# Performance work log

Hardware: AMD Instinct MI355X
Metric: run time of the kernel (lower is better)

The kernel has to match this reference:

```python
import jax, jax.numpy as jnp
import numpy as np

H = 256
V_IN = 32000
V_OUT = 32000
T = 2048


def setup_inputs() -> dict:
    key = jax.random.key(0)
    ks = jax.random.split(key, 16)
    s = 1.0 / np.sqrt(H)
    inp = {
        "src": jax.random.randint(ks[0], (T, 1), 0, V_IN, dtype=jnp.int64 if jax.config.jax_enable_x64 else jnp.int32),
        "trg": jax.random.randint(ks[1], (T, 1), 0, V_OUT, dtype=jnp.int64 if jax.config.jax_enable_x64 else jnp.int32),
        "enc_emb": jax.random.normal(ks[2], (V_IN, H), jnp.float32),
        "enc_W_ih": jax.random.uniform(ks[3], (3 * H, H), jnp.float32, -s, s),
        "enc_W_hh": jax.random.uniform(ks[4], (3 * H, H), jnp.float32, -s, s),
        "enc_b_ih": jax.random.uniform(ks[5], (3 * H,), jnp.float32, -s, s),
        "enc_b_hh": jax.random.uniform(ks[6], (3 * H,), jnp.float32, -s, s),
        "dec_emb": jax.random.normal(ks[7], (V_OUT, H), jnp.float32),
        "dec_W_ih": jax.random.uniform(ks[8], (3 * H, H), jnp.float32, -s, s),
        "dec_W_hh": jax.random.uniform(ks[9], (3 * H, H), jnp.float32, -s, s),
        "dec_b_ih": jax.random.uniform(ks[10], (3 * H,), jnp.float32, -s, s),
        "dec_b_hh": jax.random.uniform(ks[11], (3 * H,), jnp.float32, -s, s),
        "out_W": jax.random.uniform(ks[12], (V_OUT, H), jnp.float32, -s, s),
        "out_b": jax.random.uniform(ks[13], (V_OUT,), jnp.float32, -s, s),
    }
    return inp


def _gru_step(x, h, W_ih, W_hh, b_ih, b_hh):
    # PyTorch GRU cell math. x,h: [H]
    gi = W_ih @ x + b_ih          # [3H]
    gh = W_hh @ h + b_hh          # [3H]
    i_r, i_z, i_n = jnp.split(gi, 3)
    h_r, h_z, h_n = jnp.split(gh, 3)
    r = jax.nn.sigmoid(i_r + h_r)
    z = jax.nn.sigmoid(i_z + h_z)
    n = jnp.tanh(i_n + r * h_n)
    return (1.0 - z) * n + z * h


def reference(src, trg, enc_emb, enc_W_ih, enc_W_hh, enc_b_ih, enc_b_hh,
              dec_emb, dec_W_ih, dec_W_hh, dec_b_ih, dec_b_hh, out_W, out_b):
    src_t = src[:, 0]  # [T], batch forced to 1 by .view(1,1,-1)
    trg_t = trg[:, 0]  # [T]
    h0 = jnp.zeros((H,), enc_emb.dtype)

    def step(h, toks):
        s_tok, t_tok = toks
        # encoder step
        h = _gru_step(enc_emb[s_tok], h, enc_W_ih, enc_W_hh, enc_b_ih, enc_b_hh)
        # decoder step (relu on embedding per source)
        x_d = jax.nn.relu(dec_emb[t_tok])
        h = _gru_step(x_d, h, dec_W_ih, dec_W_hh, dec_b_ih, dec_b_hh)
        logits = out_W @ h + out_b          # [V_OUT]
        return h, jax.nn.log_softmax(logits)

    _, outs = jax.lax.scan(step, h0, (src_t, trg_t))
    return outs[:, None, :]  # [T, 1, V_OUT]
```

## Files before the change

kernel.cpp:

```cpp
#include <hip/hip_runtime.h>
#include <hip/hip_bf16.h>

#define T_STEPS 2048
#define HDIM 256
#define VOUT 32000

typedef short short8 __attribute__((ext_vector_type(8)));
typedef float f32x4 __attribute__((ext_vector_type(4)));

#if defined(__has_builtin)
#if __has_builtin(__builtin_amdgcn_sdot4)
#define HAVE_SDOT4 1
#endif
#if __has_builtin(__builtin_amdgcn_mov_dpp)
#define HAVE_DPP 1
#endif
#if __has_builtin(__builtin_amdgcn_rcpf)
#define HAVE_RCP 1
#endif
#endif

__device__ __forceinline__ int dot4i8(int a, int b, int c) {
#ifdef HAVE_SDOT4
    return __builtin_amdgcn_sdot4(a, b, c, false);
#else
#pragma unroll
    for (int k = 0; k < 4; ++k) {
        int av = (a << (24 - 8 * k)) >> 24;
        int bv = (b << (24 - 8 * k)) >> 24;
        c += av * bv;
    }
    return c;
#endif
}

__device__ __forceinline__ int xor1_add(int keep, int send) {
#ifdef HAVE_DPP
    return keep + __builtin_amdgcn_mov_dpp(send, 0xB1, 0xF, 0xF, true);
#else
    return keep + __shfl_xor(send, 1);
#endif
}
__device__ __forceinline__ int xor2_sum(int x) {
#ifdef HAVE_DPP
    return x + __builtin_amdgcn_mov_dpp(x, 0x4E, 0xF, 0xF, true);
#else
    return x + __shfl_xor(x, 2);
#endif
}

__device__ __forceinline__ float fast_rcp(float x) {
#ifdef HAVE_RCP
    return __builtin_amdgcn_rcpf(x);
#else
    return 1.0f / x;
#endif
}
__device__ __forceinline__ float fast_sigmoid(float x) {
    return fast_rcp(1.0f + __expf(-x));
}
__device__ __forceinline__ float fast_tanh(float x) {
    float ax = fabsf(x);
    float e = __expf(-2.0f * ax);
    float t = 1.0f - 2.0f * e * fast_rcp(1.0f + e);
    return copysignf(t, x);
}

__device__ __forceinline__ void barrier_lds() {
    asm volatile("s_waitcnt lgkmcnt(0)\n\ts_barrier" ::: "memory");
}

__global__ void k_quant(const float* __restrict__ W, int* __restrict__ wq,
                        float* __restrict__ sc) {
    int row = blockIdx.x;
    int t = threadIdx.x;
    float4 w = ((const float4*)(W + (size_t)row * HDIM))[t];
    float m = fmaxf(fmaxf(fabsf(w.x), fabsf(w.y)), fmaxf(fabsf(w.z), fabsf(w.w)));
#pragma unroll
    for (int off = 32; off; off >>= 1) m = fmaxf(m, __shfl_xor(m, off));
    float inv = (m > 0.0f) ? 127.0f / m : 0.0f;
    float scale = (m > 0.0f) ? m * (1.0f / 127.0f) : 0.0f;
    int q0 = __float2int_rn(w.x * inv); q0 = max(-127, min(127, q0));
    int q1 = __float2int_rn(w.y * inv); q1 = max(-127, min(127, q1));
    int q2 = __float2int_rn(w.z * inv); q2 = max(-127, min(127, q2));
    int q3 = __float2int_rn(w.w * inv); q3 = max(-127, min(127, q3));
    int packed = (q0 & 255) | ((q1 & 255) << 8) | ((q2 & 255) << 16) | ((q3 & 255) << 24);
    wq[row * 64 + t] = packed;
    if (t == 0) sc[row] = scale;
}

__global__ __launch_bounds__(256) void k_cvt(const float* __restrict__ in,
                                             unsigned short* __restrict__ out, int n4) {
    int i = blockIdx.x * 256 + threadIdx.x;
    if (i < n4) {
        float4 v = ((const float4*)in)[i];
        unsigned int u[4] = {__float_as_uint(v.x), __float_as_uint(v.y),
                             __float_as_uint(v.z), __float_as_uint(v.w)};
        ushort4 o;
        o.x = (unsigned short)((u[0] + 0x7FFFu + ((u[0] >> 16) & 1)) >> 16);
        o.y = (unsigned short)((u[1] + 0x7FFFu + ((u[1] >> 16) & 1)) >> 16);
        o.z = (unsigned short)((u[2] + 0x7FFFu + ((u[2] >> 16) & 1)) >> 16);
        o.w = (unsigned short)((u[3] + 0x7FFFu + ((u[3] >> 16) & 1)) >> 16);
        ((ushort4*)out)[i] = o;
    }
}

__global__ __launch_bounds__(256) void k_gi(const int* __restrict__ toks,
                                            const float* __restrict__ emb,
                                            const float* __restrict__ W,
                                            const float* __restrict__ b,
                                            const float* __restrict__ bhh,
                                            float* __restrict__ gi, int do_relu) {
    __shared__ float4 xs[64];
    int t = blockIdx.x;
    int tid = threadIdx.x;
    int tok = toks[t];
    if (tid < 64) {
        float4 x = ((const float4*)(emb + (size_t)tok * HDIM))[tid];
        if (do_relu) {
            x.x = fmaxf(x.x, 0.0f); x.y = fmaxf(x.y, 0.0f);
            x.z = fmaxf(x.z, 0.0f); x.w = fmaxf(x.w, 0.0f);
        }
        xs[tid] = x;
    }
    __syncthreads();
#pragma unroll
    for (int g = 0; g < 3; ++g) {
        int row = tid + g * 256;
        const float4* wr = (const float4*)(W + (size_t)row * HDIM);
        float acc = b[row] + ((g < 2) ? bhh[row] : 0.0f);
#pragma unroll 16
        for (int k = 0; k < 64; ++k) {
            float4 w = wr[k];
            float4 x = xs[k];
            acc += w.x * x.x + w.y * x.y + w.z * x.z + w.w * x.w;
        }
        gi[(size_t)t * 768 + row] = acc;
    }
}

__global__ __launch_bounds__(512)
__attribute__((amdgpu_waves_per_eu(2, 2))) void k_gru(
    const int* __restrict__ wq_e, const float* __restrict__ sc_e,
    const float* __restrict__ bhh_e, const float* __restrict__ gi_e,
    const int* __restrict__ wq_d, const float* __restrict__ sc_d,
    const float* __restrict__ bhh_d, const float* __restrict__ gi_d,
    unsigned short* __restrict__ h_bf) {
    __shared__ __align__(16) int HQA[64];
    __shared__ __align__(16) int HQB[64];

    const int tid = threadIdx.x;
    const int q  = tid >> 2;
    const int c  = tid & 3;
    const int el = c & 1;
    const int e  = 2 * q + el;
    const bool wr = (c & 2) == 0;

    int we[6][16], wd[6][16];
#pragma unroll
    for (int eo = 0; eo < 2; ++eo) {
#pragma unroll
        for (int g = 0; g < 3; ++g) {
            const int row = 2 * q + eo + 256 * g;
            const int4* pe = (const int4*)(wq_e + (row * 64 + c * 16));
            const int4* pd = (const int4*)(wq_d + (row * 64 + c * 16));
#pragma unroll
            for (int i = 0; i < 4; ++i) {
                int4 a = pe[i];
                we[eo * 3 + g][4 * i + 0] = a.x; we[eo * 3 + g][4 * i + 1] = a.y;
                we[eo * 3 + g][4 * i + 2] = a.z; we[eo * 3 + g][4 * i + 3] = a.w;
                int4 bq = pd[i];
                wd[eo * 3 + g][4 * i + 0] = bq.x; wd[eo * 3 + g][4 * i + 1] = bq.y;
                wd[eo * 3 + g][4 * i + 2] = bq.z; wd[eo * 3 + g][4 * i + 3] = bq.w;
            }
        }
    }
    float se0 = sc_e[e] * (1.0f / 127.0f);
    float se1 = sc_e[e + 256] * (1.0f / 127.0f);
    float se2 = sc_e[e + 512] * (1.0f / 127.0f);
    float sd0 = sc_d[e] * (1.0f / 127.0f);
    float sd1 = sc_d[e + 256] * (1.0f / 127.0f);
    float sd2 = sc_d[e + 512] * (1.0f / 127.0f);
    float be2 = bhh_e[e + 512];
    float bd2 = bhh_d[e + 512];

    float h = 0.0f;
    if (tid < 64) HQA[tid] = 0;
    __syncthreads();

    const float* ge = gi_e + e;
    const float* gd = gi_d + e;
    unsigned short* hop = h_bf + e;

    float eg0 = ge[0], eg1 = ge[256], eg2 = ge[512];

    for (int t = 0; t < T_STEPS; ++t) {
        float dg0 = gd[0], dg1 = gd[256], dg2 = gd[512];
        gd += 768;

        {
            const int4* hq4 = ((const int4*)HQA) + c * 4;
            int p[6] = {0, 0, 0, 0, 0, 0};
#pragma unroll
            for (int i = 0; i < 4; ++i) {
                int4 v = hq4[i];
#pragma unroll
                for (int j = 0; j < 6; ++j) {
                    p[j] = dot4i8(we[j][4 * i + 0], v.x, p[j]);
                    p[j] = dot4i8(we[j][4 * i + 1], v.y, p[j]);
                    p[j] = dot4i8(we[j][4 * i + 2], v.z, p[j]);
                    p[j] = dot4i8(we[j][4 * i + 3], v.w, p[j]);
                }
            }
            int f0 = xor1_add(el ? p[3] : p[0], el ? p[0] : p[3]);
            int f1 = xor1_add(el ? p[4] : p[1], el ? p[1] : p[4]);
            int f2 = xor1_add(el ? p[5] : p[2], el ? p[2] : p[5]);
            f0 = xor2_sum(f0); f1 = xor2_sum(f1); f2 = xor2_sum(f2);
            float r = fast_sigmoid(eg0 + se0 * (float)f0);
            float z = fast_sigmoid(eg1 + se1 * (float)f1);
            float n = fast_tanh(eg2 + r * (se2 * (float)f2 + be2));
            h = (1.0f - z) * n + z * h;
            if (wr)
                ((signed char*)HQB)[e] = (signed char)__float2int_rn(h * 127.0f);
        }
        barrier_lds();

        {
            const float* gen = (t < T_STEPS - 1) ? (ge + 768) : (gi_e + e);
            eg0 = gen[0]; eg1 = gen[256]; eg2 = gen[512];
            ge = gen;
        }

        {
            const int4* hq4 = ((const int4*)HQB) + c * 4;
            int p[6] = {0, 0, 0, 0, 0, 0};
#pragma unroll
            for (int i = 0; i < 4; ++i) {
                int4 v = hq4[i];
#pragma unroll
                for (int j = 0; j < 6; ++j) {
                    p[j] = dot4i8(wd[j][4 * i + 0], v.x, p[j]);
                    p[j] = dot4i8(wd[j][4 * i + 1], v.y, p[j]);
                    p[j] = dot4i8(wd[j][4 * i + 2], v.z, p[j]);
                    p[j] = dot4i8(wd[j][4 * i + 3], v.w, p[j]);
                }
            }
            int f0 = xor1_add(el ? p[3] : p[0], el ? p[0] : p[3]);
            int f1 = xor1_add(el ? p[4] : p[1], el ? p[1] : p[4]);
            int f2 = xor1_add(el ? p[5] : p[2], el ? p[2] : p[5]);
            f0 = xor2_sum(f0); f1 = xor2_sum(f1); f2 = xor2_sum(f2);
            float r = fast_sigmoid(dg0 + sd0 * (float)f0);
            float z = fast_sigmoid(dg1 + sd1 * (float)f1);
            float n = fast_tanh(dg2 + r * (sd2 * (float)f2 + bd2));
            h = (1.0f - z) * n + z * h;
            if (wr) {
                ((signed char*)HQA)[e] = (signed char)__float2int_rn(h * 127.0f);
                unsigned int u = __float_as_uint(h);
                *hop = (unsigned short)((u + 0x7FFFu + ((u >> 16) & 1)) >> 16);
            }
            hop += 256;
        }
        barrier_lds();
    }
}

__global__ __launch_bounds__(256) void k_logits(const unsigned short* __restrict__ hb,
                                                const unsigned short* __restrict__ wb,
                                                const float* __restrict__ out_b,
                                                float* __restrict__ out) {
    const int vb = blockIdx.x * 64;
    const int tb = blockIdx.y * 64;
    const int w = threadIdx.x >> 6;
    const int l = threadIdx.x & 63;
    const int m = l & 15;
    const int q = l >> 4;

    const unsigned short* aptr = hb + (size_t)(tb + w * 16 + m) * HDIM + q * 8;
    const unsigned short* bptr = wb + (size_t)(vb + m) * HDIM + q * 8;

    short8 af[8];
#pragma unroll
    for (int kt = 0; kt < 8; ++kt) af[kt] = *(const short8*)(aptr + kt * 32);

    f32x4 acc[4];
#pragma unroll
    for (int nt = 0; nt < 4; ++nt)
#pragma unroll
        for (int r = 0; r < 4; ++r) acc[nt][r] = 0.0f;

#pragma unroll
    for (int nt = 0; nt < 4; ++nt) {
        const unsigned short* bp = bptr + (size_t)nt * 16 * HDIM;
#pragma unroll
        for (int kt = 0; kt < 8; ++kt) {
            short8 bf = *(const short8*)(bp + kt * 32);
            acc[nt] = __builtin_amdgcn_mfma_f32_16x16x32_bf16(af[kt], bf, acc[nt], 0, 0, 0);
        }
    }
#pragma unroll
    for (int nt = 0; nt < 4; ++nt) {
        float bias = out_b[vb + nt * 16 + m];
#pragma unroll
        for (int r = 0; r < 4; ++r) {
            out[(size_t)(tb + w * 16 + q * 4 + r) * VOUT + vb + nt * 16 + m] =
                acc[nt][r] + bias;
        }
    }
}

__global__ __launch_bounds__(256) void k_lsesub(float* __restrict__ out) {
    const int t = blockIdx.x;
    const int tid = threadIdx.x;
    float* rowp = out + (size_t)t * VOUT;
    float m = -3.0e38f, l = 0.0f;
    for (int v = tid; v < VOUT; v += 256) {
        float x = rowp[v];
        float M = fmaxf(m, x);
        l = l * __expf(m - M) + __expf(x - M);
        m = M;
    }
#pragma unroll
    for (int off = 32; off; off >>= 1) {
        float m2 = __shfl_xor(m, off);
        float l2 = __shfl_xor(l, off);
        float M = fmaxf(m, m2);
        l = l * __expf(m - M) + l2 * __expf(m2 - M);
        m = M;
    }
    __shared__ float sm[4], sl[4];
    __shared__ float s_lse;
    int lane = tid & 63, wv = tid >> 6;
    if (lane == 0) { sm[wv] = m; sl[wv] = l; }
    __syncthreads();
    if (tid == 0) {
        float M = fmaxf(fmaxf(sm[0], sm[1]), fmaxf(sm[2], sm[3]));
        float L = sl[0] * __expf(sm[0] - M) + sl[1] * __expf(sm[1] - M) +
                  sl[2] * __expf(sm[2] - M) + sl[3] * __expf(sm[3] - M);
        s_lse = M + __logf(L);
    }
    __syncthreads();
    float s = s_lse;
    float4* p4 = (float4*)rowp;
    for (int i = tid; i < VOUT / 4; i += 256) {
        float4 o = p4[i];
        o.x -= s; o.y -= s; o.z -= s; o.w -= s;
        p4[i] = o;
    }
}

extern "C" void kernel_launch(void* const* d_in, const int* in_sizes, int n_in,
                              void* d_out, int out_size, void* d_ws, size_t ws_size,
                              hipStream_t stream) {
    (void)in_sizes; (void)n_in; (void)out_size; (void)ws_size;
    const int*   src      = (const int*)d_in[0];
    const int*   trg      = (const int*)d_in[1];
    const float* enc_emb  = (const float*)d_in[2];
    const float* enc_W_ih = (const float*)d_in[3];
    const float* enc_W_hh = (const float*)d_in[4];
    const float* enc_b_ih = (const float*)d_in[5];
    const float* enc_b_hh = (const float*)d_in[6];
    const float* dec_emb  = (const float*)d_in[7];
    const float* dec_W_ih = (const float*)d_in[8];
    const float* dec_W_hh = (const float*)d_in[9];
    const float* dec_b_ih = (const float*)d_in[10];
    const float* dec_b_hh = (const float*)d_in[11];
    const float* out_W    = (const float*)d_in[12];
    const float* out_b    = (const float*)d_in[13];
    float* out = (float*)d_out;

    char* ws = (char*)d_ws;
    float* gi_e  = (float*)ws; ws += (size_t)T_STEPS * 768 * 4;
    float* gi_d  = (float*)ws; ws += (size_t)T_STEPS * 768 * 4;
    float* sc_e  = (float*)ws; ws += 768 * 4;
    float* sc_d  = (float*)ws; ws += 768 * 4;
    int*   wq_e  = (int*)ws;   ws += 768 * 64 * 4;
    int*   wq_d  = (int*)ws;   ws += 768 * 64 * 4;
    unsigned short* h_bf = (unsigned short*)ws; ws += (size_t)T_STEPS * HDIM * 2;
    unsigned short* w_bf = (unsigned short*)ws; ws += (size_t)VOUT * HDIM * 2;

    k_quant<<<768, 64, 0, stream>>>(enc_W_hh, wq_e, sc_e);
    k_quant<<<768, 64, 0, stream>>>(dec_W_hh, wq_d, sc_d);
    k_cvt<<<(VOUT * HDIM / 4 + 255) / 256, 256, 0, stream>>>(out_W, w_bf, VOUT * HDIM / 4);
    k_gi<<<T_STEPS, 256, 0, stream>>>(src, enc_emb, enc_W_ih, enc_b_ih, enc_b_hh, gi_e, 0);
    k_gi<<<T_STEPS, 256, 0, stream>>>(trg, dec_emb, dec_W_ih, dec_b_ih, dec_b_hh, gi_d, 1);
    k_gru<<<1, 512, 0, stream>>>(wq_e, sc_e, enc_b_hh, gi_e,
                                 wq_d, sc_d, dec_b_hh, gi_d, h_bf);
    k_logits<<<dim3(VOUT / 64, T_STEPS / 64), 256, 0, stream>>>(h_bf, w_bf, out_b, out);
    k_lsesub<<<T_STEPS, 256, 0, stream>>>(out);
}
```

Measured before the change: 3.771 ms.

## Use int8 MFMA for GRU recurrent matvec with LDS gate exchange

```diff
diff --git a/kernel.cpp b/kernel.cpp
--- a/kernel.cpp
+++ b/kernel.cpp
@@ -7,47 +7,13 @@
 
 typedef short short8 __attribute__((ext_vector_type(8)));
 typedef float f32x4 __attribute__((ext_vector_type(4)));
+typedef int i32x4 __attribute__((ext_vector_type(4)));
 
 #if defined(__has_builtin)
-#if __has_builtin(__builtin_amdgcn_sdot4)
-#define HAVE_SDOT4 1
-#endif
-#if __has_builtin(__builtin_amdgcn_mov_dpp)
-#define HAVE_DPP 1
-#endif
 #if __has_builtin(__builtin_amdgcn_rcpf)
 #define HAVE_RCP 1
 #endif
 #endif
-
-__device__ __forceinline__ int dot4i8(int a, int b, int c) {
-#ifdef HAVE_SDOT4
-    return __builtin_amdgcn_sdot4(a, b, c, false);
-#else
-#pragma unroll
-    for (int k = 0; k < 4; ++k) {
-        int av = (a << (24 - 8 * k)) >> 24;
-        int bv = (b << (24 - 8 * k)) >> 24;
-        c += av * bv;
-    }
-    return c;
-#endif
-}
-
-__device__ __forceinline__ int xor1_add(int keep, int send) {
-#ifdef HAVE_DPP
-    return keep + __builtin_amdgcn_mov_dpp(send, 0xB1, 0xF, 0xF, true);
-#else
-    return keep + __shfl_xor(send, 1);
-#endif
-}
-__device__ __forceinline__ int xor2_sum(int x) {
-#ifdef HAVE_DPP
-    return x + __builtin_amdgcn_mov_dpp(x, 0x4E, 0xF, 0xF, true);
-#else
-    return x + __shfl_xor(x, 2);
-#endif
-}
 
 __device__ __forceinline__ float fast_rcp(float x) {
 #ifdef HAVE_RCP
@@ -139,58 +105,51 @@
     }
 }
 
-__global__ __launch_bounds__(512)
-__attribute__((amdgpu_waves_per_eu(2, 2))) void k_gru(
+__global__ __launch_bounds__(512, 2) void k_gru(
     const int* __restrict__ wq_e, const float* __restrict__ sc_e,
     const float* __restrict__ bhh_e, const float* __restrict__ gi_e,
     const int* __restrict__ wq_d, const float* __restrict__ sc_d,
     const float* __restrict__ bhh_d, const float* __restrict__ gi_d,
     unsigned short* __restrict__ h_bf) {
-    __shared__ __align__(16) int HQA[64];
-    __shared__ __align__(16) int HQB[64];
+    __shared__ __align__(16) int HQ[64];
+    __shared__ __align__(16) int GLDS[768];
 
     const int tid = threadIdx.x;
-    const int q  = tid >> 2;
-    const int c  = tid & 3;
-    const int el = c & 1;
-    const int e  = 2 * q + el;
-    const bool wr = (c & 2) == 0;
-
-    int we[6][16], wd[6][16];
-#pragma unroll
-    for (int eo = 0; eo < 2; ++eo) {
-#pragma unroll
-        for (int g = 0; g < 3; ++g) {
-            const int row = 2 * q + eo + 256 * g;
-            const int4* pe = (const int4*)(wq_e + (row * 64 + c * 16));
-            const int4* pd = (const int4*)(wq_d + (row * 64 + c * 16));
-#pragma unroll
-            for (int i = 0; i < 4; ++i) {
-                int4 a = pe[i];
-                we[eo * 3 + g][4 * i + 0] = a.x; we[eo * 3 + g][4 * i + 1] = a.y;
-                we[eo * 3 + g][4 * i + 2] = a.z; we[eo * 3 + g][4 * i + 3] = a.w;
-                int4 bq = pd[i];
-                wd[eo * 3 + g][4 * i + 0] = bq.x; wd[eo * 3 + g][4 * i + 1] = bq.y;
-                wd[eo * 3 + g][4 * i + 2] = bq.z; wd[eo * 3 + g][4 * i + 3] = bq.w;
-            }
-        }
-    }
-    float se0 = sc_e[e] * (1.0f / 127.0f);
-    float se1 = sc_e[e + 256] * (1.0f / 127.0f);
-    float se2 = sc_e[e + 512] * (1.0f / 127.0f);
-    float sd0 = sc_d[e] * (1.0f / 127.0f);
-    float sd1 = sc_d[e + 256] * (1.0f / 127.0f);
-    float sd2 = sc_d[e + 512] * (1.0f / 127.0f);
-    float be2 = bhh_e[e + 512];
-    float bd2 = bhh_d[e + 512];
+    const int w  = tid >> 6;
+    const int l  = tid & 63;
+    const int lr = l & 15;
+    const int lk = l >> 4;
+    const int e  = tid & 255;
+
+    i32x4 Ae[6][4], Ad[6][4];
+#pragma unroll
+    for (int j = 0; j < 6; ++j) {
+        const int row = (6 * w + j) * 16 + lr;
+#pragma unroll
+        for (int kt = 0; kt < 4; ++kt) {
+            Ae[j][kt] = *(const i32x4*)(wq_e + row * 64 + kt * 16 + lk * 4);
+            Ad[j][kt] = *(const i32x4*)(wq_d + row * 64 + kt * 16 + lk * 4);
+        }
+    }
+
+    const float se0 = sc_e[e] * (1.0f / 127.0f);
+    const float se1 = sc_e[e + 256] * (1.0f / 127.0f);
+    const float se2 = sc_e[e + 512] * (1.0f / 127.0f);
+    const float sd0 = sc_d[e] * (1.0f / 127.0f);
+    const float sd1 = sc_d[e + 256] * (1.0f / 127.0f);
+    const float sd2 = sc_d[e + 512] * (1.0f / 127.0f);
+    const float be2 = bhh_e[e + 512];
+    const float bd2 = bhh_d[e + 512];
+    const bool lead = (tid < 256);
 
     float h = 0.0f;
-    if (tid < 64) HQA[tid] = 0;
+    if (tid < 64) HQ[tid] = 0;
     __syncthreads();
 
     const float* ge = gi_e + e;
     const float* gd = gi_d + e;
     unsigned short* hop = h_bf + e;
+    const i32x4 z4 = 0;
 
     float eg0 = ge[0], eg1 = ge[256], eg2 = ge[512];
 
@@ -199,29 +158,35 @@
         gd += 768;
 
         {
-            const int4* hq4 = ((const int4*)HQA) + c * 4;
-            int p[6] = {0, 0, 0, 0, 0, 0};
-#pragma unroll
-            for (int i = 0; i < 4; ++i) {
-                int4 v = hq4[i];
-#pragma unroll
-                for (int j = 0; j < 6; ++j) {
-                    p[j] = dot4i8(we[j][4 * i + 0], v.x, p[j]);
-                    p[j] = dot4i8(we[j][4 * i + 1], v.y, p[j]);
-                    p[j] = dot4i8(we[j][4 * i + 2], v.z, p[j]);
-                    p[j] = dot4i8(we[j][4 * i + 3], v.w, p[j]);
-                }
-            }
-            int f0 = xor1_add(el ? p[3] : p[0], el ? p[0] : p[3]);
-            int f1 = xor1_add(el ? p[4] : p[1], el ? p[1] : p[4]);
-            int f2 = xor1_add(el ? p[5] : p[2], el ? p[2] : p[5]);
-            f0 = xor2_sum(f0); f1 = xor2_sum(f1); f2 = xor2_sum(f2);
-            float r = fast_sigmoid(eg0 + se0 * (float)f0);
-            float z = fast_sigmoid(eg1 + se1 * (float)f1);
-            float n = fast_tanh(eg2 + r * (se2 * (float)f2 + be2));
+            i32x4 B[4];
+#pragma unroll
+            for (int kt = 0; kt < 4; ++kt)
+                B[kt] = *(const i32x4*)(HQ + kt * 16 + lk * 4);
+            i32x4 acc[6];
+#pragma unroll
+            for (int j = 0; j < 6; ++j) {
+                i32x4 a = __builtin_amdgcn_mfma_i32_16x16x64_i8(Ae[j][0], B[0], z4, 0, 0, 0);
+                a = __builtin_amdgcn_mfma_i32_16x16x64_i8(Ae[j][1], B[1], a, 0, 0, 0);
+                a = __builtin_amdgcn_mfma_i32_16x16x64_i8(Ae[j][2], B[2], a, 0, 0, 0);
+                acc[j] = __builtin_amdgcn_mfma_i32_16x16x64_i8(Ae[j][3], B[3], a, 0, 0, 0);
+            }
+            if (lr == 0) {
+#pragma unroll
+                for (int j = 0; j < 6; ++j)
+                    *(i32x4*)(GLDS + (6 * w + j) * 16 + lk * 4) = acc[j];
+            }
+        }
+        barrier_lds();
+        {
+            float f0 = (float)GLDS[e];
+            float f1 = (float)GLDS[e + 256];
+            float f2 = (float)GLDS[e + 512];
+            float r = fast_sigmoid(eg0 + se0 * f0);
+            float z = fast_sigmoid(eg1 + se1 * f1);
+            float n = fast_tanh(eg2 + r * (se2 * f2 + be2));
             h = (1.0f - z) * n + z * h;
-            if (wr)
-                ((signed char*)HQB)[e] = (signed char)__float2int_rn(h * 127.0f);
+            if (lead)
+                ((signed char*)HQ)[e] = (signed char)__float2int_rn(h * 127.0f);
         }
         barrier_lds();
 
@@ -232,29 +197,35 @@
         }
 
         {
-            const int4* hq4 = ((const int4*)HQB) + c * 4;
-            int p[6] = {0, 0, 0, 0, 0, 0};
-#pragma unroll
-            for (int i = 0; i < 4; ++i) {
-                int4 v = hq4[i];
-#pragma unroll
-                for (int j = 0; j < 6; ++j) {
-                    p[j] = dot4i8(wd[j][4 * i + 0], v.x, p[j]);
-                    p[j] = dot4i8(wd[j][4 * i + 1], v.y, p[j]);
-                    p[j] = dot4i8(wd[j][4 * i + 2], v.z, p[j]);
-                    p[j] = dot4i8(wd[j][4 * i + 3], v.w, p[j]);
-                }
-            }
-            int f0 = xor1_add(el ? p[3] : p[0], el ? p[0] : p[3]);
-            int f1 = xor1_add(el ? p[4] : p[1], el ? p[1] : p[4]);
-            int f2 = xor1_add(el ? p[5] : p[2], el ? p[2] : p[5]);
-            f0 = xor2_sum(f0); f1 = xor2_sum(f1); f2 = xor2_sum(f2);
-            float r = fast_sigmoid(dg0 + sd0 * (float)f0);
-            float z = fast_sigmoid(dg1 + sd1 * (float)f1);
-            float n = fast_tanh(dg2 + r * (sd2 * (float)f2 + bd2));
+            i32x4 B[4];
+#pragma unroll
+            for (int kt = 0; kt < 4; ++kt)
+                B[kt] = *(const i32x4*)(HQ + kt * 16 + lk * 4);
+            i32x4 acc[6];
+#pragma unroll
+            for (int j = 0; j < 6; ++j) {
+                i32x4 a = __builtin_amdgcn_mfma_i32_16x16x64_i8(Ad[j][0], B[0], z4, 0, 0, 0);
+                a = __builtin_amdgcn_mfma_i32_16x16x64_i8(Ad[j][1], B[1], a, 0, 0, 0);
+                a = __builtin_amdgcn_mfma_i32_16x16x64_i8(Ad[j][2], B[2], a, 0, 0, 0);
+                acc[j] = __builtin_amdgcn_mfma_i32_16x16x64_i8(Ad[j][3], B[3], a, 0, 0, 0);
+            }
+            if (lr == 0) {
+#pragma unroll
+                for (int j = 0; j < 6; ++j)
+                    *(i32x4*)(GLDS + (6 * w + j) * 16 + lk * 4) = acc[j];
+            }
+        }
+        barrier_lds();
+        {
+            float f0 = (float)GLDS[e];
+            float f1 = (float)GLDS[e + 256];
+            float f2 = (float)GLDS[e + 512];
+            float r = fast_sigmoid(dg0 + sd0 * f0);
+            float z = fast_sigmoid(dg1 + sd1 * f1);
+            float n = fast_tanh(dg2 + r * (sd2 * f2 + bd2));
             h = (1.0f - z) * n + z * h;
-            if (wr) {
-                ((signed char*)HQA)[e] = (signed char)__float2int_rn(h * 127.0f);
+            if (lead) {
+                ((signed char*)HQ)[e] = (signed char)__float2int_rn(h * 127.0f);
                 unsigned int u = __float_as_uint(h);
                 *hop = (unsigned short)((u + 0x7FFFu + ((u >> 16) & 1)) >> 16);
             }
```

Measured after the change: 4.725 ms. 1.25x slower.

## Split GRU recurrent matvec between sdot4 waves and int8 MFMA waves

Applied to the files above, without the earlier changes.

```diff
diff --git a/kernel.cpp b/kernel.cpp
--- a/kernel.cpp
+++ b/kernel.cpp
@@ -7,6 +7,7 @@
 
 typedef short short8 __attribute__((ext_vector_type(8)));
 typedef float f32x4 __attribute__((ext_vector_type(4)));
+typedef int i32x4 __attribute__((ext_vector_type(4)));
 
 #if defined(__has_builtin)
 #if __has_builtin(__builtin_amdgcn_sdot4)
@@ -139,8 +140,7 @@
     }
 }
 
-__global__ __launch_bounds__(512)
-__attribute__((amdgpu_waves_per_eu(2, 2))) void k_gru(
+__global__ __launch_bounds__(512, 2) void k_gru(
     const int* __restrict__ wq_e, const float* __restrict__ sc_e,
     const float* __restrict__ bhh_e, const float* __restrict__ gi_e,
     const int* __restrict__ wq_d, const float* __restrict__ sc_d,
@@ -148,49 +148,141 @@
     unsigned short* __restrict__ h_bf) {
     __shared__ __align__(16) int HQA[64];
     __shared__ __align__(16) int HQB[64];
+    __shared__ __align__(16) int GLDS[384];
 
     const int tid = threadIdx.x;
-    const int q  = tid >> 2;
+    const bool isV = tid < 256;
+    const int l  = tid & 63;
+    const int lr = l & 15;
+    const int lk = l >> 4;
     const int c  = tid & 3;
-    const int el = c & 1;
-    const int e  = 2 * q + el;
-    const bool wr = (c & 2) == 0;
-
-    int we[6][16], wd[6][16];
-#pragma unroll
-    for (int eo = 0; eo < 2; ++eo) {
-#pragma unroll
-        for (int g = 0; g < 3; ++g) {
-            const int row = 2 * q + eo + 256 * g;
-            const int4* pe = (const int4*)(wq_e + (row * 64 + c * 16));
-            const int4* pd = (const int4*)(wq_d + (row * 64 + c * 16));
-#pragma unroll
-            for (int i = 0; i < 4; ++i) {
-                int4 a = pe[i];
-                we[eo * 3 + g][4 * i + 0] = a.x; we[eo * 3 + g][4 * i + 1] = a.y;
-                we[eo * 3 + g][4 * i + 2] = a.z; we[eo * 3 + g][4 * i + 3] = a.w;
-                int4 bq = pd[i];
-                wd[eo * 3 + g][4 * i + 0] = bq.x; wd[eo * 3 + g][4 * i + 1] = bq.y;
-                wd[eo * 3 + g][4 * i + 2] = bq.z; wd[eo * 3 + g][4 * i + 3] = bq.w;
-            }
-        }
-    }
-    float se0 = sc_e[e] * (1.0f / 127.0f);
-    float se1 = sc_e[e + 256] * (1.0f / 127.0f);
-    float se2 = sc_e[e + 512] * (1.0f / 127.0f);
-    float sd0 = sc_d[e] * (1.0f / 127.0f);
-    float sd1 = sc_d[e + 256] * (1.0f / 127.0f);
-    float sd2 = sc_d[e + 512] * (1.0f / 127.0f);
-    float be2 = bhh_e[e + 512];
-    float bd2 = bhh_d[e + 512];
+    const int el = tid & 1;
+
+    const int eidx = isV ? (2 * (tid >> 2) + el) : (128 + ((tid - 256) & 127));
+    const bool duty = isV ? ((tid & 2) == 0) : (tid < 384);
+
+    i32x4 WE[6][4], WD[6][4];
+    int goff[6];
+    if (isV) {
+        const int q = tid >> 2;
+#pragma unroll
+        for (int eo = 0; eo < 2; ++eo)
+#pragma unroll
+            for (int g = 0; g < 3; ++g) {
+                const int row = 2 * q + eo + 256 * g;
+                const int j = eo * 3 + g;
+#pragma unroll
+                for (int i = 0; i < 4; ++i) {
+                    WE[j][i] = *(const i32x4*)(wq_e + row * 64 + c * 16 + i * 4);
+                    WD[j][i] = *(const i32x4*)(wq_d + row * 64 + c * 16 + i * 4);
+                }
+                goff[j] = 0;
+            }
+    } else {
+        const int mw = (tid >> 6) - 4;
+#pragma unroll
+        for (int tj = 0; tj < 6; ++tj) {
+            const int TJ = mw * 6 + tj;
+            const int g = TJ >> 3, s = TJ & 7;
+            const int row = 256 * g + 128 + 16 * s + lr;
+#pragma unroll
+            for (int kt = 0; kt < 4; ++kt) {
+                WE[tj][kt] = *(const i32x4*)(wq_e + row * 64 + kt * 16 + lk * 4);
+                WD[tj][kt] = *(const i32x4*)(wq_d + row * 64 + kt * 16 + lk * 4);
+            }
+            goff[tj] = g * 128 + 16 * s + lk * 4;
+        }
+    }
+
+    const float se0 = sc_e[eidx] * (1.0f / 127.0f);
+    const float se1 = sc_e[eidx + 256] * (1.0f / 127.0f);
+    const float se2 = sc_e[eidx + 512] * (1.0f / 127.0f);
+    const float sd0 = sc_d[eidx] * (1.0f / 127.0f);
+    const float sd1 = sc_d[eidx + 256] * (1.0f / 127.0f);
+    const float sd2 = sc_d[eidx + 512] * (1.0f / 127.0f);
+    const float be2 = bhh_e[eidx + 512];
+    const float bd2 = bhh_d[eidx + 512];
 
     float h = 0.0f;
     if (tid < 64) HQA[tid] = 0;
     __syncthreads();
 
-    const float* ge = gi_e + e;
-    const float* gd = gi_d + e;
-    unsigned short* hop = h_bf + e;
+    const float* ge = gi_e + eidx;
+    const float* gd = gi_d + eidx;
+    unsigned short* hop = h_bf + eidx;
+    const i32x4 z4 = {0, 0, 0, 0};
+
+    auto half = [&](const i32x4(&W)[6][4], float g0, float g1, float g2,
+                    float s0, float s1, float s2, float bn,
+                    const int* HQr, int* HQw, unsigned short* hout) {
+        if (isV) {
+            const int4* hq4 = ((const int4*)HQr) + c * 4;
+            int p0 = 0, p1 = 0, p2 = 0, p3 = 0, p4 = 0, p5 = 0;
+#pragma unroll
+            for (int i = 0; i < 4; ++i) {
+                int4 v = hq4[i];
+                p0 = dot4i8(W[0][i][0], v.x, p0); p0 = dot4i8(W[0][i][1], v.y, p0);
+                p0 = dot4i8(W[0][i][2], v.z, p0); p0 = dot4i8(W[0][i][3], v.w, p0);
+                p1 = dot4i8(W[1][i][0], v.x, p1); p1 = dot4i8(W[1][i][1], v.y, p1);
+                p1 = dot4i8(W[1][i][2], v.z, p1); p1 = dot4i8(W[1][i][3], v.w, p1);
+                p2 = dot4i8(W[2][i][0], v.x, p2); p2 = dot4i8(W[2][i][1], v.y, p2);
+                p2 = dot4i8(W[2][i][2], v.z, p2); p2 = dot4i8(W[2][i][3], v.w, p2);
+                p3 = dot4i8(W[3][i][0], v.x, p3); p3 = dot4i8(W[3][i][1], v.y, p3);
+                p3 = dot4i8(W[3][i][2], v.z, p3); p3 = dot4i8(W[3][i][3], v.w, p3);
+                p4 = dot4i8(W[4][i][0], v.x, p4); p4 = dot4i8(W[4][i][1], v.y, p4);
+                p4 = dot4i8(W[4][i][2], v.z, p4); p4 = dot4i8(W[4][i][3], v.w, p4);
+                p5 = dot4i8(W[5][i][0], v.x, p5); p5 = dot4i8(W[5][i][1], v.y, p5);
+                p5 = dot4i8(W[5][i][2], v.z, p5); p5 = dot4i8(W[5][i][3], v.w, p5);
+            }
+            int f0 = xor1_add(el ? p3 : p0, el ? p0 : p3);
+            int f1 = xor1_add(el ? p4 : p1, el ? p1 : p4);
+            int f2 = xor1_add(el ? p5 : p2, el ? p2 : p5);
+            f0 = xor2_sum(f0); f1 = xor2_sum(f1); f2 = xor2_sum(f2);
+            float r = fast_sigmoid(g0 + s0 * (float)f0);
+            float z = fast_sigmoid(g1 + s1 * (float)f1);
+            float n = fast_tanh(g2 + r * (s2 * (float)f2 + bn));
+            h = (1.0f - z) * n + z * h;
+            if (duty) {
+                ((signed char*)HQw)[eidx] = (signed char)__float2int_rn(h * 127.0f);
+                if (hout) {
+                    unsigned int u = __float_as_uint(h);
+                    *hout = (unsigned short)((u + 0x7FFFu + ((u >> 16) & 1)) >> 16);
+                }
+            }
+            barrier_lds();
+            barrier_lds();
+        } else {
+            i32x4 B0 = *(const i32x4*)(HQr + 0 * 16 + lk * 4);
+            i32x4 B1 = *(const i32x4*)(HQr + 1 * 16 + lk * 4);
+            i32x4 B2 = *(const i32x4*)(HQr + 2 * 16 + lk * 4);
+            i32x4 B3 = *(const i32x4*)(HQr + 3 * 16 + lk * 4);
+#pragma unroll
+            for (int tj = 0; tj < 6; ++tj) {
+                i32x4 a = __builtin_amdgcn_mfma_i32_16x16x64_i8(W[tj][0], B0, z4, 0, 0, 0);
+                a = __builtin_amdgcn_mfma_i32_16x16x64_i8(W[tj][1], B1, a, 0, 0, 0);
+                a = __builtin_amdgcn_mfma_i32_16x16x64_i8(W[tj][2], B2, a, 0, 0, 0);
+                a = __builtin_amdgcn_mfma_i32_16x16x64_i8(W[tj][3], B3, a, 0, 0, 0);
+                if (lr == 0) *(i32x4*)(GLDS + goff[tj]) = a;
+            }
+            barrier_lds();
+            const int ep = eidx - 128;
+            float f0 = (float)GLDS[ep];
+            float f1 = (float)GLDS[128 + ep];
+            float f2 = (float)GLDS[256 + ep];
+            float r = fast_sigmoid(g0 + s0 * f0);
+            float z = fast_sigmoid(g1 + s1 * f1);
+            float n = fast_tanh(g2 + r * (s2 * f2 + bn));
+            h = (1.0f - z) * n + z * h;
+            if (duty) {
+                ((signed char*)HQw)[eidx] = (signed char)__float2int_rn(h * 127.0f);
+                if (hout) {
+                    unsigned int u = __float_as_uint(h);
+                    *hout = (unsigned short)((u + 0x7FFFu + ((u >> 16) & 1)) >> 16);
+                }
+            }
+            barrier_lds();
+        }
+    };
 
     float eg0 = ge[0], eg1 = ge[256], eg2 = ge[512];
 
@@ -198,69 +290,16 @@
         float dg0 = gd[0], dg1 = gd[256], dg2 = gd[512];
         gd += 768;
 
+        half(WE, eg0, eg1, eg2, se0, se1, se2, be2, HQA, HQB, nullptr);
+
         {
-            const int4* hq4 = ((const int4*)HQA) + c * 4;
-            int p[6] = {0, 0, 0, 0, 0, 0};
-#pragma unroll
-            for (int i = 0; i < 4; ++i) {
-                int4 v = hq4[i];
-#pragma unroll
-                for (int j = 0; j < 6; ++j) {
-                    p[j] = dot4i8(we[j][4 * i + 0], v.x, p[j]);
-                    p[j] = dot4i8(we[j][4 * i + 1], v.y, p[j]);
-                    p[j] = dot4i8(we[j][4 * i + 2], v.z, p[j]);
-                    p[j] = dot4i8(we[j][4 * i + 3], v.w, p[j]);
-                }
-            }
-            int f0 = xor1_add(el ? p[3] : p[0], el ? p[0] : p[3]);
-            int f1 = xor1_add(el ? p[4] : p[1], el ? p[1] : p[4]);
-            int f2 = xor1_add(el ? p[5] : p[2], el ? p[2] : p[5]);
-            f0 = xor2_sum(f0); f1 = xor2_sum(f1); f2 = xor2_sum(f2);
-            float r = fast_sigmoid(eg0 + se0 * (float)f0);
-            float z = fast_sigmoid(eg1 + se1 * (float)f1);
-            float n = fast_tanh(eg2 + r * (se2 * (float)f2 + be2));
-            h = (1.0f - z) * n + z * h;
-            if (wr)
-                ((signed char*)HQB)[e] = (signed char)__float2int_rn(h * 127.0f);
-        }
-        barrier_lds();
-
-        {
-            const float* gen = (t < T_STEPS - 1) ? (ge + 768) : (gi_e + e);
+            const float* gen = (t < T_STEPS - 1) ? (ge + 768) : (gi_e + eidx);
             eg0 = gen[0]; eg1 = gen[256]; eg2 = gen[512];
             ge = gen;
         }
 
-        {
-            const int4* hq4 = ((const int4*)HQB) + c * 4;
-            int p[6] = {0, 0, 0, 0, 0, 0};
-#pragma unroll
-            for (int i = 0; i < 4; ++i) {
-                int4 v = hq4[i];
-#pragma unroll
-                for (int j = 0; j < 6; ++j) {
-                    p[j] = dot4i8(wd[j][4 * i + 0], v.x, p[j]);
-                    p[j] = dot4i8(wd[j][4 * i + 1], v.y, p[j]);
-                    p[j] = dot4i8(wd[j][4 * i + 2], v.z, p[j]);
-                    p[j] = dot4i8(wd[j][4 * i + 3], v.w, p[j]);
-                }
-            }
-            int f0 = xor1_add(el ? p[3] : p[0], el ? p[0] : p[3]);
-            int f1 = xor1_add(el ? p[4] : p[1], el ? p[1] : p[4]);
-            int f2 = xor1_add(el ? p[5] : p[2], el ? p[2] : p[5]);
-            f0 = xor2_sum(f0); f1 = xor2_sum(f1); f2 = xor2_sum(f2);
-            float r = fast_sigmoid(dg0 + sd0 * (float)f0);
-            float z = fast_sigmoid(dg1 + sd1 * (float)f1);
-            float n = fast_tanh(dg2 + r * (sd2 * (float)f2 + bd2));
-            h = (1.0f - z) * n + z * h;
-            if (wr) {
-                ((signed char*)HQA)[e] = (signed char)__float2int_rn(h * 127.0f);
-                unsigned int u = __float_as_uint(h);
-                *hop = (unsigned short)((u + 0x7FFFu + ((u >> 16) & 1)) >> 16);
-            }
-            hop += 256;
-        }
-        barrier_lds();
+        half(WD, dg0, dg1, dg2, sd0, sd1, sd2, bd2, HQB, HQA, hop);
+        hop += 256;
     }
 }
 
```

New measurement: 4.402 ms. +16.7%, slower.
